# Performance work log

Measured on AMD Instinct MI355X. Metric: run time of the kernel, lower is better.

Reference implementation:

```python
import jax, jax.numpy as jnp
import numpy as np

MODEL_DIM = 1024
HEADS = 16
HEAD_DIM = MODEL_DIM // HEADS
B, T = 2, 2048
TB_LEN = 500  # time_bias table length


def setup_inputs() -> dict:
    key = jax.random.key(0)
    ks = jax.random.split(key, 12)
    s = 0.02
    d = MODEL_DIM
    return {
        "x": jax.random.normal(ks[0], (B, T, d), dtype=jnp.float32),
        "Wq": jax.random.normal(ks[1], (d, d), dtype=jnp.float32) * s,
        "bq": jnp.zeros((d,), jnp.float32),
        "Wk": jax.random.normal(ks[2], (d, d), dtype=jnp.float32) * s,
        "bk": jnp.zeros((d,), jnp.float32),
        "Wv": jax.random.normal(ks[3], (d, d), dtype=jnp.float32) * s,
        "bv": jnp.zeros((d,), jnp.float32),
        "Wo": jax.random.normal(ks[4], (d, d), dtype=jnp.float32) * s,
        "bo": jnp.zeros((d,), jnp.float32),
        "et_gate": jax.random.normal(ks[5], (1, 1, 1), dtype=jnp.float32),
        "is_gate": jax.random.normal(ks[6], (1, 1, 1), dtype=jnp.float32),
        "time_bias": jnp.linspace(-1.0, 1.0, TB_LEN, dtype=jnp.float32).reshape(1, 1, TB_LEN),
    }


def reference(x, Wq, bq, Wk, bk, Wv, bv, Wo, bo, et_gate, is_gate, time_bias):
    Bb, Tt, D = x.shape
    H, hd = HEADS, HEAD_DIM
    # projections (torch Linear: y = x @ W.T + b), split heads -> [B,H,T,hd]
    Q = (x @ Wq.T + bq).reshape(Bb, Tt, H, hd).transpose(0, 2, 1, 3)
    K = (x @ Wk.T + bk).reshape(Bb, Tt, H, hd).transpose(0, 2, 1, 3)
    V = (x @ Wv.T + bv).reshape(Bb, Tt, H, hd).transpose(0, 2, 1, 3)
    scores = jnp.einsum("bhqd,bhkd->bhqk", Q, K) / jnp.sqrt(jnp.float32(hd))
    # relative-position gather from the fixed time-bias table
    pos = jnp.arange(Tt)[None, :] - jnp.arange(Tt)[:, None]          # [T,T]
    idx = jnp.clip(pos + TB_LEN // 2, 0, TB_LEN - 1)                 # [T,T]
    tp = time_bias[:, :, idx]                                        # [1,1,T,T]
    tp = jnp.squeeze(tp, axis=1)[None, None]                         # [1,1,1,T,T] (faithful to torch)
    # broadcast: [B,H,T,T] + [1,1,1,T,T] -> [1,B,H,T,T] (faithful 5-D scores)
    scores = scores + jax.nn.sigmoid(et_gate) * tp + is_gate
    attn = jax.nn.softmax(scores, axis=-1)                           # [1,B,H,T,T]
    context = jnp.matmul(attn, V)                                    # [1,B,H,T,hd]
    # faithful torch transpose(1,2).reshape(B,T,D) on the 5-D tensor
    context = context.transpose(0, 2, 1, 3, 4).reshape(Bb, Tt, D)
    return context @ Wo.T + bo
```

## Files before the change

### kernel.cpp

```cpp
#include <hip/hip_runtime.h>

typedef __bf16 bf16_t;
typedef __bf16 bf16x4 __attribute__((ext_vector_type(4)));
typedef __bf16 bf16x8 __attribute__((ext_vector_type(8)));
typedef float f32x4 __attribute__((ext_vector_type(4)));

__device__ __forceinline__ f32x4 mfma16(bf16x8 a, bf16x8 b, f32x4 c) {
    return __builtin_amdgcn_mfma_f32_16x16x32_bf16(a, b, c, 0, 0, 0);
}

__device__ __forceinline__ void gload16(bf16_t* lds, const bf16_t* g) {
    __builtin_amdgcn_global_load_lds(
        (const __attribute__((address_space(1))) void*)g,
        (__attribute__((address_space(3))) void*)lds, 16, 0, 0);
}

#define TRD(dst, base, OFFSTR)                                          \
    asm volatile("ds_read_b64_tr_b16 %0, %1 offset:" OFFSTR             \
                 : "=v"(dst)                                            \
                 : "v"((const __attribute__((address_space(3))) bf16_t*)(base)))

__device__ __forceinline__ float ex2(float x) {
    float r;
    asm("v_exp_f32 %0, %1" : "=v"(r) : "v"(x));
    return r;
}

__global__ __launch_bounds__(256) void cvt_all(
    const float* __restrict__ x,
    const float* __restrict__ w0, const float* __restrict__ w1,
    const float* __restrict__ w2, const float* __restrict__ w3,
    bf16_t* __restrict__ xb, bf16_t* __restrict__ o0, bf16_t* __restrict__ o1,
    bf16_t* __restrict__ o2, bf16_t* __restrict__ o3) {
    const int bid = blockIdx.x;
    const float* in;
    bf16_t* out;
    int off;
    if (bid < 4096) {
        in = x; out = xb; off = bid;
    } else {
        const int wsel = (bid - 4096) >> 10;
        off = (bid - 4096) & 1023;
        if (wsel == 0) { in = w0; out = o0; }
        else if (wsel == 1) { in = w1; out = o1; }
        else if (wsel == 2) { in = w2; out = o2; }
        else { in = w3; out = o3; }
    }
    const int i = (off * 256 + threadIdx.x) * 4;
    float4 v = *reinterpret_cast<const float4*>(in + i);
    bf16x4 o = {(bf16_t)v.x, (bf16_t)v.y, (bf16_t)v.z, (bf16_t)v.w};
    *reinterpret_cast<bf16x4*>(out + i) = o;
}

template <typename OutT>
__device__ __forceinline__ void gemm_tile(bf16_t (*As)[4096], bf16_t (*Bs)[4096],
                                          const bf16_t* A, const bf16_t* B,
                                          const float* bias, OutT* C,
                                          int M, int N, int K, int bx, int by,
                                          float scale) {
    const int tid = threadIdx.x;
    const int l = tid & 63, w = tid >> 6;
    const int lr = l & 15, lg = l >> 4;
    const int wr = (w >> 1) * 32, wc = (w & 1) * 64;
    const int m0 = bx * 128, n0 = by * 128;

    f32x4 acc[2][4];
#pragma unroll
    for (int m = 0; m < 2; ++m)
#pragma unroll
        for (int n = 0; n < 4; ++n) acc[m][n] = (f32x4)0.f;

    const int rA = tid >> 2, cA = (tid & 3) * 8;
    const bf16_t* ga = A + (size_t)(m0 + rA) * K + cA;
    const bf16_t* gb = B + (size_t)(n0 + rA) * K + cA;

    auto stage = [&](int buf) {
        gload16(As[buf] + tid * 8, ga);
        gload16(Bs[buf] + tid * 8, gb);
        ga += 32; gb += 32;
    };

    stage(0);
    stage(1);
    const int NT = K >> 5;
    int cur = 0, n2 = 2;
    for (int t = 0; t < NT; ++t) {
        if (t < NT - 1) asm volatile("s_waitcnt vmcnt(2)" ::: "memory");
        else asm volatile("s_waitcnt vmcnt(0)" ::: "memory");
        __builtin_amdgcn_sched_barrier(0);
        __builtin_amdgcn_s_barrier();
        __builtin_amdgcn_sched_barrier(0);
        if (t + 2 < NT) stage(n2);

        bf16x8 af[2], bfr[4];
#pragma unroll
        for (int m = 0; m < 2; ++m)
            af[m] = *reinterpret_cast<bf16x8*>(As[cur] + (wr + m * 16 + lr) * 32 + lg * 8);
#pragma unroll
        for (int n = 0; n < 4; ++n)
            bfr[n] = *reinterpret_cast<bf16x8*>(Bs[cur] + (wc + n * 16 + lr) * 32 + lg * 8);
#pragma unroll
        for (int m = 0; m < 2; ++m)
#pragma unroll
            for (int n = 0; n < 4; ++n)
                acc[m][n] = mfma16(af[m], bfr[n], acc[m][n]);

        cur = (cur == 2) ? 0 : cur + 1;
        n2 = (n2 == 2) ? 0 : n2 + 1;
    }
#pragma unroll
    for (int m = 0; m < 2; ++m) {
        const int row = m0 + wr + m * 16 + lg * 4;
#pragma unroll
        for (int n = 0; n < 4; ++n) {
            const int col = n0 + wc + n * 16 + lr;
            const float bv = bias[col];
#pragma unroll
            for (int j = 0; j < 4; ++j) {
                float v = (acc[m][n][j] + bv) * scale;
                C[(size_t)(row + j) * N + col] = (OutT)v;
            }
        }
    }
}

template <typename OutT>
__global__ __launch_bounds__(512, 4) void gemm_bt(const bf16_t* __restrict__ A,
                                                  const bf16_t* __restrict__ B,
                                                  const float* __restrict__ bias,
                                                  OutT* __restrict__ C,
                                                  int M, int N, int K) {
    __shared__ bf16_t As[3][4096];
    __shared__ bf16_t Bs[3][4096];
    gemm_tile<OutT>(As, Bs, A, B, bias, C, M, N, K, blockIdx.x, blockIdx.y, 1.f);
}

__global__ __launch_bounds__(512, 4) void gemm_qkv(
    const bf16_t* __restrict__ A,
    const bf16_t* W0, const bf16_t* W1, const bf16_t* W2,
    const float* b0, const float* b1, const float* b2,
    bf16_t* C0, bf16_t* C1, bf16_t* C2) {
    __shared__ bf16_t As[3][4096];
    __shared__ bf16_t Bs[3][4096];
    const bf16_t* B = W0; const float* bias = b0; bf16_t* C = C0;
    float scale = 0.1803368801111204f;
    if (blockIdx.z == 1) { B = W1; bias = b1; C = C1; scale = 1.f; }
    else if (blockIdx.z == 2) { B = W2; bias = b2; C = C2; scale = 1.f; }
    gemm_tile<bf16_t>(As, Bs, A, B, bias, C, 4096, 1024, 1024,
                      blockIdx.x, blockIdx.y, scale);
}

__global__ __launch_bounds__(256, 4) void attn_fused(
    const bf16_t* __restrict__ Qb, const bf16_t* __restrict__ Kb,
    const bf16_t* __restrict__ Vb, bf16_t* __restrict__ Cx,
    const float* __restrict__ time_bias, const float* __restrict__ et_gate) {
    constexpr int T = 2048;
    constexpr int D = 1024;
    __shared__ bf16_t Kl[3][4096];
    __shared__ bf16_t Vl[2][4096];
    const int tid = threadIdx.x;
    const int w = tid >> 6, l = tid & 63;
    const int lr = l & 15, lg = l >> 4;
    const int flat = blockIdx.x;
    const int xcd = flat & 7, idx = flat >> 3;
    const int bh = (xcd << 2) | (idx >> 5);
    const int qt = idx & 31;
    const int b = bh >> 4, h = bh & 15;
    const size_t bT = (size_t)b * T;
    const int h64 = h * 64;

    const float sig = 1.f / (1.f + __expf(-et_gate[0]));
    const float slope = (time_bias[499] - time_bias[0]) * (1.f / 499.f);
    const float c1 = sig * slope * 1.4426950408889634f;
    const float C499 = c1 * 499.f;

    const int q0 = qt * 64 + w * 16;
    const bf16_t* qbase = Qb + (bT + q0 + lr) * D + h64;
    bf16x8 qf0 = *reinterpret_cast<const bf16x8*>(qbase + lg * 8);
    bf16x8 qf1 = *reinterpret_cast<const bf16x8*>(qbase + 32 + lg * 8);

    const int r0 = tid >> 3, d80 = ((tid & 7) ^ (r0 & 7)) << 3;
    const int q1i = tid + 256;
    const int r1 = q1i >> 3, d81 = ((q1i & 7) ^ (r1 & 7)) << 3;
    const bf16_t* kg0 = Kb + (bT + r0) * D + h64 + d80;
    const bf16_t* kg1 = Kb + (bT + r1) * D + h64 + d81;
    const int kv0v = ((tid >> 5) << 2) + ((tid >> 1) & 3);
    const int dd0 = (((tid >> 3) & 3) << 4) + ((tid & 1) << 3);
    const int kv1v = ((q1i >> 5) << 2) + ((q1i >> 1) & 3);
    const int dd1 = (((q1i >> 3) & 3) << 4) + ((q1i & 1) << 3);
    const bf16_t* vg0 = Vb + (bT + kv0v) * D + h64 + dd0;
    const bf16_t* vg1 = Vb + (bT + kv1v) * D + h64 + dd1;

    auto stageK = [&](int buf) {
        gload16(&Kl[buf][tid * 8], kg0);
        gload16(&Kl[buf][(tid + 256) * 8], kg1);
        kg0 += 64 * D; kg1 += 64 * D;
    };
    auto stageV = [&](int buf) {
        gload16(&Vl[buf][tid * 8], vg0);
        gload16(&Vl[buf][(tid + 256) * 8], vg1);
        vg0 += 64 * D; vg1 += 64 * D;
    };

    f32x4 acc[4];
#pragma unroll
    for (int n = 0; n < 4; ++n) acc[n] = (f32x4)0.f;
    f32x4 acc_li = (f32x4)0.f;
    bf16x8 onesf;
#pragma unroll
    for (int e = 0; e < 8; ++e) onesf[e] = (bf16_t)1.f;
    f32x4 zero4 = (f32x4)0.f;

    float tb_lane = (float)(250 - q0 - lr + lg * 4);

    stageK(0);
    stageV(0);
    stageK(1);

    const uint32_t swz = (uint32_t)(lr & 7) << 4;
    const uint32_t koffA = (uint32_t)(lr * 128) + (((uint32_t)(lg * 16)) ^ swz);
    const uint32_t koffB = (uint32_t)(lr * 128) + (((uint32_t)(64 + lg * 16)) ^ swz);
    const int voff = lg * 256 + lr * 4;

    int kcur = 0, vcur = 0;

    for (int t = 0; t < 32; ++t) {
        if (t < 31) asm volatile("s_waitcnt vmcnt(2)" ::: "memory");
        else asm volatile("s_waitcnt vmcnt(0)" ::: "memory");
        __builtin_amdgcn_sched_barrier(0);
        __builtin_amdgcn_s_barrier();
        __builtin_amdgcn_sched_barrier(0);
        if (t + 1 < 32) stageV(vcur ^ 1);
        if (t + 2 < 32) stageK(kcur == 0 ? 2 : kcur - 1);

        const char* Kc = (const char*)Kl[kcur];
        const char* Ka = Kc + koffA;
        const char* Kb2 = Kc + koffB;

        f32x4 s[4];
        __builtin_amdgcn_s_setprio(1);
#pragma unroll
        for (int n = 0; n < 4; ++n) {
            bf16x8 kf0 = *reinterpret_cast<const bf16x8*>(Ka + n * 2048);
            bf16x8 kf1 = *reinterpret_cast<const bf16x8*>(Kb2 + n * 2048);
            s[n] = mfma16(kf0, qf0, zero4);
            s[n] = mfma16(kf1, qf1, s[n]);
        }
        __builtin_amdgcn_s_setprio(0);

        const int base = 250 - q0 + t * 64;
        if (base >= 15 && base <= 436) {
#pragma unroll
            for (int n = 0; n < 4; ++n)
#pragma unroll
                for (int j = 0; j < 4; ++j) {
                    const float x = tb_lane + (float)(n * 16 + j);
                    s[n][j] = ex2(fmaf(c1, x, s[n][j]));
                }
        } else if (base + 63 <= 0) {
#pragma unroll
            for (int n = 0; n < 4; ++n)
#pragma unroll
                for (int j = 0; j < 4; ++j) s[n][j] = ex2(s[n][j]);
        } else if (base >= 514) {
#pragma unroll
            for (int n = 0; n < 4; ++n)
#pragma unroll
                for (int j = 0; j < 4; ++j) s[n][j] = ex2(s[n][j] + C499);
        } else {
#pragma unroll
            for (int n = 0; n < 4; ++n)
#pragma unroll
                for (int j = 0; j < 4; ++j) {
                    float x = tb_lane + (float)(n * 16 + j);
                    x = fminf(fmaxf(x, 0.f), 499.f);
                    s[n][j] = ex2(fmaf(c1, x, s[n][j]));
                }
        }
        tb_lane += 64.f;

        bf16x8 pf0, pf1;
#pragma unroll
        for (int j = 0; j < 4; ++j) {
            pf0[j] = (bf16_t)s[0][j];
            pf0[4 + j] = (bf16_t)s[1][j];
            pf1[j] = (bf16_t)s[2][j];
            pf1[4 + j] = (bf16_t)s[3][j];
        }

        const bf16_t* vb2 = Vl[vcur] + voff;
        bf16x4 vlo[8], vhi[8];
        TRD(vlo[0], vb2, "0");    TRD(vhi[0], vb2, "2048");
        TRD(vlo[1], vb2, "4096"); TRD(vhi[1], vb2, "6144");
        TRD(vlo[2], vb2, "128");  TRD(vhi[2], vb2, "2176");
        TRD(vlo[3], vb2, "4224"); TRD(vhi[3], vb2, "6272");
        TRD(vlo[4], vb2, "256");  TRD(vhi[4], vb2, "2304");
        TRD(vlo[5], vb2, "4352"); TRD(vhi[5], vb2, "6400");
        TRD(vlo[6], vb2, "384");  TRD(vhi[6], vb2, "2432");
        TRD(vlo[7], vb2, "4480"); TRD(vhi[7], vb2, "6528");

        __builtin_amdgcn_s_setprio(1);
        acc_li = mfma16(pf0, onesf, acc_li);
        acc_li = mfma16(pf1, onesf, acc_li);

        asm volatile("s_waitcnt lgkmcnt(8)" ::: "memory");
        __builtin_amdgcn_sched_barrier(0);
#pragma unroll
        for (int i2 = 0; i2 < 4; ++i2) {
            bf16x8 vf = __builtin_shufflevector(vlo[i2], vhi[i2],
                                                0, 1, 2, 3, 4, 5, 6, 7);
            acc[i2 >> 1] = mfma16((i2 & 1) ? pf1 : pf0, vf, acc[i2 >> 1]);
        }
        asm volatile("s_waitcnt lgkmcnt(0)" ::: "memory");
        __builtin_amdgcn_sched_barrier(0);
#pragma unroll
        for (int i2 = 4; i2 < 8; ++i2) {
            bf16x8 vf = __builtin_shufflevector(vlo[i2], vhi[i2],
                                                0, 1, 2, 3, 4, 5, 6, 7);
            acc[i2 >> 1] = mfma16((i2 & 1) ? pf1 : pf0, vf, acc[i2 >> 1]);
        }
        __builtin_amdgcn_s_setprio(0);
        __builtin_amdgcn_sched_barrier(0);

        kcur = (kcur == 2) ? 0 : kcur + 1;
        vcur ^= 1;
    }

#pragma unroll
    for (int j = 0; j < 4; ++j) {
        const float invj = __builtin_amdgcn_rcpf(acc_li[j]);
        const int tq = q0 + lg * 4 + j;
        const size_t base_o = ((size_t)(h * 2 + b) * T + tq) * 64;
#pragma unroll
        for (int n = 0; n < 4; ++n)
            Cx[base_o + n * 16 + lr] = (bf16_t)(acc[n][j] * invj);
    }
}

extern "C" void kernel_launch(void* const* d_in, const int* in_sizes, int n_in,
                              void* d_out, int out_size, void* d_ws, size_t ws_size,
                              hipStream_t stream) {
    (void)in_sizes; (void)n_in; (void)out_size; (void)ws_size;
    const float* x  = (const float*)d_in[0];
    const float* Wq = (const float*)d_in[1];
    const float* bq = (const float*)d_in[2];
    const float* Wk = (const float*)d_in[3];
    const float* bk = (const float*)d_in[4];
    const float* Wv = (const float*)d_in[5];
    const float* bv = (const float*)d_in[6];
    const float* Wo = (const float*)d_in[7];
    const float* bo = (const float*)d_in[8];
    const float* et = (const float*)d_in[9];
    const float* tb = (const float*)d_in[11];

    char* ws = (char*)d_ws;
    const size_t MB = 1 << 20;
    bf16_t* xb  = (bf16_t*)(ws + 0 * MB);
    bf16_t* wqb = (bf16_t*)(ws + 8 * MB);
    bf16_t* wkb = (bf16_t*)(ws + 10 * MB);
    bf16_t* wvb = (bf16_t*)(ws + 12 * MB);
    bf16_t* wob = (bf16_t*)(ws + 14 * MB);
    bf16_t* Qb  = (bf16_t*)(ws + 16 * MB);
    bf16_t* Kb  = (bf16_t*)(ws + 24 * MB);
    bf16_t* Vb  = (bf16_t*)(ws + 32 * MB);
    bf16_t* Cx  = (bf16_t*)(ws + 40 * MB);

    cvt_all<<<8192, 256, 0, stream>>>(x, Wq, Wk, Wv, Wo, xb, wqb, wkb, wvb, wob);

    gemm_qkv<<<dim3(32, 8, 3), 512, 0, stream>>>(xb, wqb, wkb, wvb,
                                                 bq, bk, bv, Qb, Kb, Vb);

    attn_fused<<<1024, 256, 0, stream>>>(Qb, Kb, Vb, Cx, tb, et);

    gemm_bt<float><<<dim3(32, 8), 512, 0, stream>>>(Cx, wob, bo, (float*)d_out,
                                                    4096, 1024, 1024);
}
```

Before: 116.9 us.

## Software-pipeline QK^T one tile ahead of softmax and PV in attention loop

Restructures the attention main loop so the QK^T MFMAs for the next key tile are issued at the end of the current iteration. Each iteration then starts by issuing the V transposed LDS reads and the next global-to-LDS stages, and runs the exp/bias math while those reads are in flight. The waits are reworked: one lgkmcnt(0) before the PV MFMAs replaces the split waits, and the vmcnt counts are retuned. The goal is to hide LDS and global-load latency behind the exponent work. The risk is that the next K tile is read from LDS after only a per-thread vmcnt wait with no workgroup barrier, so rows loaded by other threads may not be visible yet. Register pressure also rises.

```diff
diff --git a/kernel.cpp b/kernel.cpp
--- a/kernel.cpp
+++ b/kernel.cpp
@@ -213,32 +213,24 @@
 
     float tb_lane = (float)(250 - q0 - lr + lg * 4);
 
-    stageK(0);
-    stageV(0);
-    stageK(1);
-
     const uint32_t swz = (uint32_t)(lr & 7) << 4;
     const uint32_t koffA = (uint32_t)(lr * 128) + (((uint32_t)(lg * 16)) ^ swz);
     const uint32_t koffB = (uint32_t)(lr * 128) + (((uint32_t)(64 + lg * 16)) ^ swz);
     const int voff = lg * 256 + lr * 4;
 
-    int kcur = 0, vcur = 0;
-
-    for (int t = 0; t < 32; ++t) {
-        if (t < 31) asm volatile("s_waitcnt vmcnt(2)" ::: "memory");
-        else asm volatile("s_waitcnt vmcnt(0)" ::: "memory");
-        __builtin_amdgcn_sched_barrier(0);
-        __builtin_amdgcn_s_barrier();
-        __builtin_amdgcn_sched_barrier(0);
-        if (t + 1 < 32) stageV(vcur ^ 1);
-        if (t + 2 < 32) stageK(kcur == 0 ? 2 : kcur - 1);
-
-        const char* Kc = (const char*)Kl[kcur];
+    stageK(0);
+    stageV(0);
+    stageK(1);
+    asm volatile("s_waitcnt vmcnt(2)" ::: "memory");
+    __builtin_amdgcn_sched_barrier(0);
+    __builtin_amdgcn_s_barrier();
+    __builtin_amdgcn_sched_barrier(0);
+
+    f32x4 s[4];
+    {
+        const char* Kc = (const char*)Kl[0];
         const char* Ka = Kc + koffA;
         const char* Kb2 = Kc + koffB;
-
-        f32x4 s[4];
-        __builtin_amdgcn_s_setprio(1);
 #pragma unroll
         for (int n = 0; n < 4; ++n) {
             bf16x8 kf0 = *reinterpret_cast<const bf16x8*>(Ka + n * 2048);
@@ -246,49 +238,16 @@
             s[n] = mfma16(kf0, qf0, zero4);
             s[n] = mfma16(kf1, qf1, s[n]);
         }
-        __builtin_amdgcn_s_setprio(0);
-
-        const int base = 250 - q0 + t * 64;
-        if (base >= 15 && base <= 436) {
-#pragma unroll
-            for (int n = 0; n < 4; ++n)
-#pragma unroll
-                for (int j = 0; j < 4; ++j) {
-                    const float x = tb_lane + (float)(n * 16 + j);
-                    s[n][j] = ex2(fmaf(c1, x, s[n][j]));
-                }
-        } else if (base + 63 <= 0) {
-#pragma unroll
-            for (int n = 0; n < 4; ++n)
-#pragma unroll
-                for (int j = 0; j < 4; ++j) s[n][j] = ex2(s[n][j]);
-        } else if (base >= 514) {
-#pragma unroll
-            for (int n = 0; n < 4; ++n)
-#pragma unroll
-                for (int j = 0; j < 4; ++j) s[n][j] = ex2(s[n][j] + C499);
-        } else {
-#pragma unroll
-            for (int n = 0; n < 4; ++n)
-#pragma unroll
-                for (int j = 0; j < 4; ++j) {
-                    float x = tb_lane + (float)(n * 16 + j);
-                    x = fminf(fmaxf(x, 0.f), 499.f);
-                    s[n][j] = ex2(fmaf(c1, x, s[n][j]));
-                }
-        }
-        tb_lane += 64.f;
-
-        bf16x8 pf0, pf1;
-#pragma unroll
-        for (int j = 0; j < 4; ++j) {
-            pf0[j] = (bf16_t)s[0][j];
-            pf0[4 + j] = (bf16_t)s[1][j];
-            pf1[j] = (bf16_t)s[2][j];
-            pf1[4 + j] = (bf16_t)s[3][j];
-        }
-
-        const bf16_t* vb2 = Vl[vcur] + voff;
+    }
+
+    for (int t = 0; t < 32; ++t) {
+        if (t < 31) asm volatile("s_waitcnt vmcnt(1)" ::: "memory");
+        else asm volatile("s_waitcnt vmcnt(0)" ::: "memory");
+        __builtin_amdgcn_sched_barrier(0);
+        __builtin_amdgcn_s_barrier();
+        __builtin_amdgcn_sched_barrier(0);
+
+        const bf16_t* vb2 = Vl[t & 1] + voff;
         bf16x4 vlo[8], vhi[8];
         TRD(vlo[0], vb2, "0");    TRD(vhi[0], vb2, "2048");
         TRD(vlo[1], vb2, "4096"); TRD(vhi[1], vb2, "6144");
@@ -299,31 +258,78 @@
         TRD(vlo[6], vb2, "384");  TRD(vhi[6], vb2, "2432");
         TRD(vlo[7], vb2, "4480"); TRD(vhi[7], vb2, "6528");
 
+        if (t + 1 < 32) stageV((t + 1) & 1);
+        if (t + 2 < 32) stageK((t + 2) % 3);
+
+        const int base = 250 - q0 + t * 64;
+        if (base >= 15 && base <= 436) {
+#pragma unroll
+            for (int n = 0; n < 4; ++n)
+#pragma unroll
+                for (int j = 0; j < 4; ++j) {
+                    const float x = tb_lane + (float)(n * 16 + j);
+                    s[n][j] = ex2(fmaf(c1, x, s[n][j]));
+                }
+        } else if (base + 63 <= 0) {
+#pragma unroll
+            for (int n = 0; n < 4; ++n)
+#pragma unroll
+                for (int j = 0; j < 4; ++j) s[n][j] = ex2(s[n][j]);
+        } else if (base >= 514) {
+#pragma unroll
+            for (int n = 0; n < 4; ++n)
+#pragma unroll
+                for (int j = 0; j < 4; ++j) s[n][j] = ex2(s[n][j] + C499);
+        } else {
+#pragma unroll
+            for (int n = 0; n < 4; ++n)
+#pragma unroll
+                for (int j = 0; j < 4; ++j) {
+                    float x = tb_lane + (float)(n * 16 + j);
+                    x = fminf(fmaxf(x, 0.f), 499.f);
+                    s[n][j] = ex2(fmaf(c1, x, s[n][j]));
+                }
+        }
+        tb_lane += 64.f;
+
+        bf16x8 pf0, pf1;
+#pragma unroll
+        for (int j = 0; j < 4; ++j) {
+            pf0[j] = (bf16_t)s[0][j];
+            pf0[4 + j] = (bf16_t)s[1][j];
+            pf1[j] = (bf16_t)s[2][j];
+            pf1[4 + j] = (bf16_t)s[3][j];
+        }
+
+        asm volatile("s_waitcnt lgkmcnt(0)" ::: "memory");
+        __builtin_amdgcn_sched_barrier(0);
         __builtin_amdgcn_s_setprio(1);
         acc_li = mfma16(pf0, onesf, acc_li);
         acc_li = mfma16(pf1, onesf, acc_li);
-
-        asm volatile("s_waitcnt lgkmcnt(8)" ::: "memory");
-        __builtin_amdgcn_sched_barrier(0);
-#pragma unroll
-        for (int i2 = 0; i2 < 4; ++i2) {
+#pragma unroll
+        for (int i2 = 0; i2 < 8; ++i2) {
             bf16x8 vf = __builtin_shufflevector(vlo[i2], vhi[i2],
                                                 0, 1, 2, 3, 4, 5, 6, 7);
             acc[i2 >> 1] = mfma16((i2 & 1) ? pf1 : pf0, vf, acc[i2 >> 1]);
         }
-        asm volatile("s_waitcnt lgkmcnt(0)" ::: "memory");
-        __builtin_amdgcn_sched_barrier(0);
-#pragma unroll
-        for (int i2 = 4; i2 < 8; ++i2) {
-            bf16x8 vf = __builtin_shufflevector(vlo[i2], vhi[i2],
-                                                0, 1, 2, 3, 4, 5, 6, 7);
-            acc[i2 >> 1] = mfma16((i2 & 1) ? pf1 : pf0, vf, acc[i2 >> 1]);
+
+        if (t + 1 < 32) {
+            if (t < 30) asm volatile("s_waitcnt vmcnt(2)" ::: "memory");
+            else asm volatile("s_waitcnt vmcnt(1)" ::: "memory");
+            __builtin_amdgcn_sched_barrier(0);
+            const char* Kc = (const char*)Kl[(t + 1) % 3];
+            const char* Ka = Kc + koffA;
+            const char* Kb2 = Kc + koffB;
+#pragma unroll
+            for (int n = 0; n < 4; ++n) {
+                bf16x8 kf0 = *reinterpret_cast<const bf16x8*>(Ka + n * 2048);
+                bf16x8 kf1 = *reinterpret_cast<const bf16x8*>(Kb2 + n * 2048);
+                s[n] = mfma16(kf0, qf0, zero4);
+                s[n] = mfma16(kf1, qf1, s[n]);
+            }
         }
         __builtin_amdgcn_s_setprio(0);
         __builtin_amdgcn_sched_barrier(0);
-
-        kcur = (kcur == 2) ? 0 : kcur + 1;
-        vcur ^= 1;
     }
 
 #pragma unroll
```

Result: no change. 116.4 us (-0.4%).
